# Kernel optimization log

Hardware: AMD Instinct MI355X
Metric: run time of the kernel (lower is better)

## Reference

```python
import jax, jax.numpy as jnp
import numpy as np
import math

HEADS = 32
GROUPS = 8
HEAD_DIM = 64
HIDDEN = 2048
B, S = 2, 2048


def _rope(x, freqs_cis):
    # x: (..., S, head_dim); freqs_cis: (S, head_dim) -> interleaved cos/sin pattern
    x_even = x[..., ::2]
    x_odd = x[..., 1::2]
    cos = freqs_cis[..., ::2]
    sin = freqs_cis[..., 1::2]
    r_even = x_even * cos - x_odd * sin
    r_odd = x_even * sin + x_odd * cos
    return jnp.stack([r_even, r_odd], axis=-1).reshape(x.shape)


def setup_inputs() -> dict:
    key = jax.random.key(0)
    ks = jax.random.split(key, 12)
    scale = 1.0 / math.sqrt(HIDDEN)
    x = jax.random.normal(ks[0], (B, S, HIDDEN), dtype=jnp.float32)
    freqs_cis = jax.random.uniform(ks[1], (S, HEAD_DIM), dtype=jnp.float32)
    causal = jnp.tril(jnp.ones((S, S), dtype=bool))
    mask = jnp.where(causal, 0.0, -1e9).astype(jnp.float32)
    kv_dims = HEAD_DIM * GROUPS
    wq = jax.random.normal(ks[2], (HIDDEN, HIDDEN), jnp.float32) * scale
    bq = jnp.zeros((HIDDEN,), jnp.float32)
    wk = jax.random.normal(ks[3], (kv_dims, HIDDEN), jnp.float32) * scale
    bk = jnp.zeros((kv_dims,), jnp.float32)
    wv = jax.random.normal(ks[4], (kv_dims, HIDDEN), jnp.float32) * scale
    bv = jnp.zeros((kv_dims,), jnp.float32)
    wo = jax.random.normal(ks[5], (HIDDEN, HIDDEN), jnp.float32) * scale
    bo = jnp.zeros((HIDDEN,), jnp.float32)
    return dict(x=x, freqs_cis=freqs_cis, mask=mask, wq=wq, bq=bq,
                wk=wk, bk=bk, wv=wv, bv=bv, wo=wo, bo=bo)


def reference(x, freqs_cis, mask, wq, bq, wk, bk, wv, bv, wo, bo):
    b, s, h = x.shape
    rep = HEADS // GROUPS
    q = x @ wq.T + bq                      # (B,S,H)
    k = x @ wk.T + bk                      # (B,S,G*hd)
    v = x @ wv.T + bv
    q = q.reshape(b, s, HEADS, HEAD_DIM).transpose(0, 2, 1, 3)   # (B,Hh,S,hd)
    k = k.reshape(b, s, GROUPS, HEAD_DIM).transpose(0, 2, 1, 3)  # (B,G,S,hd)
    v = v.reshape(b, s, GROUPS, HEAD_DIM).transpose(0, 2, 1, 3)
    q = _rope(q, freqs_cis)
    k = _rope(k, freqs_cis)
    # GQA: group q heads instead of materially repeating K/V
    qg = q.reshape(b, GROUPS, rep, s, HEAD_DIM)
    scores = jnp.einsum('bgrsd,bgtd->bgrst', qg, k) / math.sqrt(HEAD_DIM)
    scores = scores + mask                 # broadcast (S,S)
    attn = jax.nn.softmax(scores, axis=-1)
    out = jnp.einsum('bgrst,bgtd->bgrsd', attn, v)
    out = out.reshape(b, HEADS, s, HEAD_DIM).transpose(0, 2, 1, 3).reshape(b, s, h)
    return out @ wo.T + bo
```

## Files before the change

### kernel.cpp

```cpp
#include <hip/hip_runtime.h>

#define S_LEN 2048
#define HID   2048
#define NQH   32
#define NKV   8
#define HD    64

typedef __bf16 bf16x8 __attribute__((ext_vector_type(8)));
typedef __bf16 bf16x4 __attribute__((ext_vector_type(4)));
typedef float  f32x4  __attribute__((ext_vector_type(4)));

#define MFMA16(a, b, c) __builtin_amdgcn_mfma_f32_16x16x32_bf16(a, b, c, 0, 0, 0)

__device__ __forceinline__ void async_copy16(const void* g, void* l) {
  __builtin_amdgcn_global_load_lds(
      (const __attribute__((address_space(1))) unsigned int*)g,
      (__attribute__((address_space(3))) unsigned int*)l, 16, 0, 0);
}

__global__ void cast_all_k(const float* __restrict__ x,  const float* __restrict__ wq,
                           const float* __restrict__ wk, const float* __restrict__ wv,
                           const float* __restrict__ wo,
                           __bf16* __restrict__ xb,  __bf16* __restrict__ wqb,
                           __bf16* __restrict__ wkb, __bf16* __restrict__ wvb,
                           __bf16* __restrict__ wob) {
  int bid = blockIdx.x;
  const float* in; __bf16* out; int base;
  if (bid < 8192)       { in = x;  out = xb;  base = bid; }
  else if (bid < 12288) { in = wq; out = wqb; base = bid - 8192; }
  else if (bid < 13312) { in = wk; out = wkb; base = bid - 12288; }
  else if (bid < 14336) { in = wv; out = wvb; base = bid - 13312; }
  else                  { in = wo; out = wob; base = bid - 14336; }
  int i = (base * 256 + threadIdx.x) * 4;
  float4 v = *(const float4*)(in + i);
  bf16x4 o;
  o[0] = (__bf16)v.x; o[1] = (__bf16)v.y; o[2] = (__bf16)v.z; o[3] = (__bf16)v.w;
  *(bf16x4*)(out + i) = o;
}

__device__ __forceinline__ void gemm_core(const __bf16* __restrict__ A, const __bf16* __restrict__ B,
                                          int m0, int n0, int K,
                                          __bf16 (&Asm)[128][32], __bf16 (&Bsm)[128][32],
                                          f32x4 (&acc)[4][4]) {
  const int tid = threadIdx.x, wave = tid >> 6, lane = tid & 63;
  const int l15 = lane & 15, quad = lane >> 4;
  const int wr = wave >> 1, wc = wave & 1;
  const int lrow = lane >> 2, lcol = (lane & 3) * 8;

  const __bf16* ag = A + (size_t)(m0 + wave * 32 + lrow) * K + lcol;
  const __bf16* bg = B + (size_t)(n0 + wave * 32 + lrow) * K + lcol;
  __bf16* al = &Asm[wave * 32][0];
  __bf16* bl = &Bsm[wave * 32][0];
  const size_t rowstep = (size_t)16 * K;

  for (int kt = 0; kt < K; kt += 32) {
    __syncthreads();
    async_copy16(ag + kt, al);
    async_copy16(ag + kt + rowstep, al + 16 * 32);
    async_copy16(bg + kt, bl);
    async_copy16(bg + kt + rowstep, bl + 16 * 32);
    __syncthreads();
    bf16x8 af[4], bfr[4];
#pragma unroll
    for (int mt = 0; mt < 4; mt++)
      af[mt] = *(const bf16x8*)&Asm[wr * 64 + mt * 16 + l15][quad * 8];
#pragma unroll
    for (int nt = 0; nt < 4; nt++)
      bfr[nt] = *(const bf16x8*)&Bsm[wc * 64 + nt * 16 + l15][quad * 8];
#pragma unroll
    for (int mt = 0; mt < 4; mt++)
#pragma unroll
      for (int nt = 0; nt < 4; nt++)
        acc[mt][nt] = MFMA16(af[mt], bfr[nt], acc[mt][nt]);
  }
}

__global__ __launch_bounds__(256) void gemm_qkv_k(const __bf16* __restrict__ xb,
    const __bf16* __restrict__ wqb, const __bf16* __restrict__ wkb, const __bf16* __restrict__ wvb,
    const float* __restrict__ bq, const float* __restrict__ bk, const float* __restrict__ bv,
    const float* __restrict__ fr,
    __bf16* __restrict__ Qb, __bf16* __restrict__ Kb, __bf16* __restrict__ Vt) {
  __shared__ __align__(16) __bf16 Asm[128][32];
  __shared__ __align__(16) __bf16 Bsm[128][32];
  const int by = blockIdx.y;
  const int m0 = blockIdx.x * 128;
  const __bf16* B; const float* bias; int n0;
  int mode;
  if (by < 16)      { B = wqb; bias = bq; n0 = by * 128;        mode = 0; }
  else if (by < 20) { B = wkb; bias = bk; n0 = (by - 16) * 128; mode = 1; }
  else              { B = wvb; bias = bv; n0 = (by - 20) * 128; mode = 2; }

  f32x4 acc[4][4] = {};
  gemm_core(xb, B, m0, n0, HID, Asm, Bsm, acc);

  const int tid = threadIdx.x, wave = tid >> 6, lane = tid & 63;
  const int l15 = lane & 15, quad = lane >> 4;
  const int wr = wave >> 1, wc = wave & 1;

  if (mode == 2) {
#pragma unroll
    for (int nt = 0; nt < 4; nt++) {
      int col = n0 + wc * 64 + nt * 16 + l15;
      int g = col >> 6, d = col & 63;
      float bv2 = bias[col];
#pragma unroll
      for (int mt = 0; mt < 4; mt++) {
        int row = m0 + wr * 64 + mt * 16 + quad * 4;
        int b = row >> 11, s = row & 2047;
        bf16x4 o;
#pragma unroll
        for (int r = 0; r < 4; r++) o[r] = (__bf16)(acc[mt][nt][r] + bv2);
        *(bf16x4*)(Vt + (((size_t)(b * NKV + g) * HD + d)) * S_LEN + s) = o;
      }
    }
  } else {
    const float scale = (mode == 0) ? 0.125f * 1.44269504f : 1.0f;
    const int ldc = (mode == 0) ? HID : 512;
    __bf16* C = (mode == 0) ? Qb : Kb;
    const int dpar = l15 & 1;
#pragma unroll
    for (int nt = 0; nt < 4; nt++) {
      int col = n0 + wc * 64 + nt * 16 + l15;
      int d = col & 63;
      float bv2 = bias[col];
#pragma unroll
      for (int mt = 0; mt < 4; mt++) {
        int row = m0 + wr * 64 + mt * 16 + quad * 4;
        int s = row & 2047;
#pragma unroll
        for (int r = 0; r < 4; r++) {
          float v = acc[mt][nt][r] + bv2;
          float p = __shfl_xor(v, 1, 64);
          float f = fr[(size_t)(s + r) * HD + d];
          float fp = __shfl_xor(f, 1, 64);
          float o = dpar ? (p * f + v * fp) : (v * f - p * fp);
          C[(size_t)(row + r) * ldc + col] = (__bf16)(o * scale);
        }
      }
    }
  }
}

__global__ __launch_bounds__(256) void gemm_out_k(const __bf16* __restrict__ A,
    const __bf16* __restrict__ Bw, const float* __restrict__ bias, float* __restrict__ C) {
  __shared__ __align__(16) __bf16 Asm[128][32];
  __shared__ __align__(16) __bf16 Bsm[128][32];
  const int m0 = blockIdx.x * 128, n0 = blockIdx.y * 128;
  f32x4 acc[4][4] = {};
  gemm_core(A, Bw, m0, n0, HID, Asm, Bsm, acc);
  const int tid = threadIdx.x, wave = tid >> 6, lane = tid & 63;
  const int l15 = lane & 15, quad = lane >> 4;
  const int wr = wave >> 1, wc = wave & 1;
#pragma unroll
  for (int nt = 0; nt < 4; nt++) {
    int col = n0 + wc * 64 + nt * 16 + l15;
    float bv = bias[col];
#pragma unroll
    for (int mt = 0; mt < 4; mt++) {
      int row = m0 + wr * 64 + mt * 16 + quad * 4;
#pragma unroll
      for (int r = 0; r < 4; r++)
        C[(size_t)(row + r) * HID + col] = acc[mt][nt][r] + bv;
    }
  }
}

__global__ __launch_bounds__(256, 4) void flash_k(const __bf16* __restrict__ Q,
                                                  const __bf16* __restrict__ K,
                                                  const __bf16* __restrict__ Vt,
                                                  __bf16* __restrict__ O) {
  __shared__ __align__(64) __bf16 Ksm[64][64];
  __shared__ __align__(64) __bf16 Vsm[64][64];
  __shared__ __align__(64) __bf16 Psm[4][16][64];
  const int tid = threadIdx.x;
  const int wave = tid >> 6, lane = tid & 63;
  const int l15 = lane & 15, quad = lane >> 4;
  const int x7 = l15 & 7, l15h = l15 >> 3;
  const int bh = blockIdx.x;
  const int b = bh >> 5, h = bh & 31, g = h >> 2;

  const int srow = tid >> 2, sc = (tid & 3) * 16;
  const int r7 = srow & 7;
  const int w0 = (((sc >> 3))     ^ r7) * 8;
  const int w1 = (((sc >> 3) + 1) ^ r7) * 8;

  char* kbp = (char*)&Ksm[0][0];
  char* vbp = (char*)&Vsm[0][0];
  char* pbp = (char*)&Psm[0][0][0];
  int kr[2], pr[2], pw[4];
#pragma unroll
  for (int ks = 0; ks < 2; ks++) {
    kr[ks] = l15 * 128 + (((ks * 4 + quad) ^ x7) * 16);
    pr[ks] = wave * 2048 + kr[ks];
  }
#pragma unroll
  for (int nt = 0; nt < 4; nt++)
    pw[nt] = wave * 2048 + quad * 512 + x7 * 2 + (((2 * nt + l15h) ^ ((quad & 1) * 4)) * 16);

  bf16x8 ones;
#pragma unroll
  for (int j = 0; j < 8; j++) ones[j] = (__bf16)1.0f;

  const __bf16* kbase = K + ((size_t)b * S_LEN + srow) * (NKV * HD) + g * HD + sc;
  const __bf16* vbase = Vt + (((size_t)b * NKV + g) * HD + srow) * S_LEN + sc;

#pragma unroll 1
  for (int half = 0; half < 2; half++) {
    const int qt = half ? (31 - (int)blockIdx.y) : (int)blockIdx.y;
    const int wq0 = qt * 64 + wave * 16;

    const __bf16* qp = Q + ((size_t)(b * S_LEN + wq0 + l15)) * HID + h * HD + quad * 8;
    bf16x8 qf0 = *(const bf16x8*)qp;
    bf16x8 qf1 = *(const bf16x8*)(qp + 32);

    f32x4 acc[4] = {};
    f32x4 accs = {};

    const __bf16* kp = kbase;
    const __bf16* vp = vbase;
    uint4 k0 = *(const uint4*)kp, k1 = *(const uint4*)(kp + 8);
    uint4 v0 = *(const uint4*)vp, v1 = *(const uint4*)(vp + 8);

    for (int t = 0; t <= qt; t++) {
      const int kv0 = t * 64;
      __syncthreads();
      *(uint4*)&Ksm[srow][w0] = k0;
      *(uint4*)&Ksm[srow][w1] = k1;
      *(uint4*)&Vsm[srow][w0] = v0;
      *(uint4*)&Vsm[srow][w1] = v1;
      if (t < qt) {
        kp += 64 * NKV * HD;  vp += 64;
        k0 = *(const uint4*)kp; k1 = *(const uint4*)(kp + 8);
        v0 = *(const uint4*)vp; v1 = *(const uint4*)(vp + 8);
      }
      __syncthreads();

      if (kv0 > wq0 + 15) continue;

      bf16x8 kf[2][4];
#pragma unroll
      for (int ks = 0; ks < 2; ks++)
#pragma unroll
        for (int nt = 0; nt < 4; nt++)
          kf[ks][nt] = *(const bf16x8*)(kbp + (kr[ks] + nt * 2048));

      f32x4 sacc[4] = {};
#pragma unroll
      for (int nt = 0; nt < 4; nt++) {
        sacc[nt] = MFMA16(qf0, kf[0][nt], sacc[nt]);
        sacc[nt] = MFMA16(qf1, kf[1][nt], sacc[nt]);
      }
      const bool domask = (kv0 + 63 > wq0);
#pragma unroll
      for (int nt = 0; nt < 4; nt++) {
        int kv = kv0 + nt * 16 + l15;
        int qr = wq0 + quad * 4;
#pragma unroll
        for (int r = 0; r < 4; r++) {
          float p = __builtin_exp2f(sacc[nt][r]);
          if (domask && kv > qr + r) p = 0.f;
          *(__bf16*)(pbp + ((pw[nt] ^ (r << 4)) + r * 128)) = (__bf16)p;
        }
      }

#pragma unroll
      for (int ks = 0; ks < 2; ks++) {
        bf16x8 vf[4];
#pragma unroll
        for (int nt = 0; nt < 4; nt++)
          vf[nt] = *(const bf16x8*)(vbp + (kr[ks] + nt * 2048));
        bf16x8 pf = *(const bf16x8*)(pbp + pr[ks]);
        accs = MFMA16(pf, ones, accs);
#pragma unroll
        for (int nt = 0; nt < 4; nt++)
          acc[nt] = MFMA16(pf, vf[nt], acc[nt]);
      }
    }

    __bf16* op = O + ((size_t)(b * S_LEN + wq0 + quad * 4)) * HID + h * HD;
    float inv[4];
#pragma unroll
    for (int r = 0; r < 4; r++) inv[r] = 1.f / accs[r];
#pragma unroll
    for (int nt = 0; nt < 4; nt++)
#pragma unroll
      for (int r = 0; r < 4; r++)
        op[(size_t)r * HID + nt * 16 + l15] = (__bf16)(acc[nt][r] * inv[r]);
  }
}

extern "C" void kernel_launch(void* const* d_in, const int* in_sizes, int n_in,
                              void* d_out, int out_size, void* d_ws, size_t ws_size,
                              hipStream_t stream) {
  (void)in_sizes; (void)n_in; (void)out_size; (void)ws_size;
  const float* x  = (const float*)d_in[0];
  const float* fr = (const float*)d_in[1];
  const float* wq = (const float*)d_in[3];
  const float* bq = (const float*)d_in[4];
  const float* wk = (const float*)d_in[5];
  const float* bk = (const float*)d_in[6];
  const float* wv = (const float*)d_in[7];
  const float* bv = (const float*)d_in[8];
  const float* wo = (const float*)d_in[9];
  const float* bo = (const float*)d_in[10];
  float* out = (float*)d_out;
  char* ws = (char*)d_ws;

  __bf16* xb  = (__bf16*)(ws);
  __bf16* wqb = (__bf16*)(ws + ((size_t)16 << 20));
  __bf16* wkb = (__bf16*)(ws + ((size_t)24 << 20));
  __bf16* wvb = (__bf16*)(ws + ((size_t)26 << 20));
  __bf16* wob = (__bf16*)(ws + ((size_t)28 << 20));
  __bf16* Qb  = (__bf16*)(ws + ((size_t)36 << 20));
  __bf16* Kb  = (__bf16*)(ws + ((size_t)52 << 20));
  __bf16* Vtb = (__bf16*)(ws + ((size_t)60 << 20));
  __bf16* Ab  = (__bf16*)(ws + ((size_t)64 << 20));

  cast_all_k<<<18432, 256, 0, stream>>>(x, wq, wk, wv, wo, xb, wqb, wkb, wvb, wob);

  gemm_qkv_k<<<dim3(32, 24), 256, 0, stream>>>(xb, wqb, wkb, wvb, bq, bk, bv, fr, Qb, Kb, Vtb);

  flash_k<<<dim3(64, 16), 256, 0, stream>>>(Qb, Kb, Vtb, Ab);

  gemm_out_k<<<dim3(32, 16), 256, 0, stream>>>(Ab, wob, bo, out);
}
```

Before: 341.9 us.

## Triple-buffer GEMM loads with swizzled LDS and larger 256x128 tiles

Replaces the single-buffered 128x128x32 GEMM core with a three-stage async global-to-LDS pipeline using 256x128x64 tiles, 512-thread blocks, XOR-swizzled LDS columns to avoid bank conflicts, and s_setprio around the MFMA block. Both the QKV projection and output projection kernels use the new core, with halved grid in M. The aim is to hide global load latency behind MFMA work and reduce barrier overhead per K step. The risk is higher LDS use (about 144KB per block) limiting occupancy, and fewer blocks (384 and 256) against the CU count.

```diff
diff --git a/kernel.cpp b/kernel.cpp
--- a/kernel.cpp
+++ b/kernel.cpp
@@ -5,6 +5,10 @@
 #define NQH   32
 #define NKV   8
 #define HD    64
+
+#define BM 256
+#define BN 128
+#define BK 64
 
 typedef __bf16 bf16x8 __attribute__((ext_vector_type(8)));
 typedef __bf16 bf16x4 __attribute__((ext_vector_type(4)));
@@ -38,52 +42,88 @@
   *(bf16x4*)(out + i) = o;
 }
 
-__device__ __forceinline__ void gemm_core(const __bf16* __restrict__ A, const __bf16* __restrict__ B,
+__device__ __forceinline__ void gemm_pipe(const __bf16* __restrict__ A,
+                                          const __bf16* __restrict__ B,
                                           int m0, int n0, int K,
-                                          __bf16 (&Asm)[128][32], __bf16 (&Bsm)[128][32],
+                                          __bf16 (&As)[3][BM][BK],
+                                          __bf16 (&Bs)[3][BN][BK],
                                           f32x4 (&acc)[4][4]) {
   const int tid = threadIdx.x, wave = tid >> 6, lane = tid & 63;
   const int l15 = lane & 15, quad = lane >> 4;
   const int wr = wave >> 1, wc = wave & 1;
-  const int lrow = lane >> 2, lcol = (lane & 3) * 8;
-
-  const __bf16* ag = A + (size_t)(m0 + wave * 32 + lrow) * K + lcol;
-  const __bf16* bg = B + (size_t)(n0 + wave * 32 + lrow) * K + lcol;
-  __bf16* al = &Asm[wave * 32][0];
-  __bf16* bl = &Bsm[wave * 32][0];
-  const size_t rowstep = (size_t)16 * K;
-
-  for (int kt = 0; kt < K; kt += 32) {
-    __syncthreads();
-    async_copy16(ag + kt, al);
-    async_copy16(ag + kt + rowstep, al + 16 * 32);
-    async_copy16(bg + kt, bl);
-    async_copy16(bg + kt + rowstep, bl + 16 * 32);
-    __syncthreads();
-    bf16x8 af[4], bfr[4];
-#pragma unroll
-    for (int mt = 0; mt < 4; mt++)
-      af[mt] = *(const bf16x8*)&Asm[wr * 64 + mt * 16 + l15][quad * 8];
-#pragma unroll
-    for (int nt = 0; nt < 4; nt++)
-      bfr[nt] = *(const bf16x8*)&Bsm[wc * 64 + nt * 16 + l15][quad * 8];
-#pragma unroll
-    for (int mt = 0; mt < 4; mt++)
-#pragma unroll
-      for (int nt = 0; nt < 4; nt++)
-        acc[mt][nt] = MFMA16(af[mt], bfr[nt], acc[mt][nt]);
-  }
-}
-
-__global__ __launch_bounds__(256) void gemm_qkv_k(const __bf16* __restrict__ xb,
+
+  const int srow = lane >> 3;
+  const int scol = ((lane & 7) ^ srow) * 8;
+  const __bf16* ga = A + (size_t)(m0 + wave * 32 + srow) * K + scol;
+  const __bf16* gb = B + (size_t)(n0 + wave * 16 + srow) * K + scol;
+
+  const int c0 = ((quad)     ^ (l15 & 7)) * 8;
+  const int c1 = ((4 + quad) ^ (l15 & 7)) * 8;
+
+  const int NT = K / BK;
+
+#define STAGE(st, kt) do {                                                        \
+    _Pragma("unroll")                                                             \
+    for (int i = 0; i < 4; i++)                                                   \
+      async_copy16(ga + (kt) + (size_t)(i * 8) * K, &As[st][wave * 32 + i * 8][0]); \
+    _Pragma("unroll")                                                             \
+    for (int i = 0; i < 2; i++)                                                   \
+      async_copy16(gb + (kt) + (size_t)(i * 8) * K, &Bs[st][wave * 16 + i * 8][0]); \
+  } while (0)
+
+  STAGE(0, 0);
+  STAGE(1, BK);
+
+  int s = 0;
+  for (int t = 0; t < NT; t++) {
+    if (t + 1 < NT) asm volatile("s_waitcnt vmcnt(6) lgkmcnt(0)" ::: "memory");
+    else            asm volatile("s_waitcnt vmcnt(0) lgkmcnt(0)" ::: "memory");
+    __builtin_amdgcn_s_barrier();
+    asm volatile("" ::: "memory");
+
+    if (t + 2 < NT) {
+      int s2 = s + 2; if (s2 >= 3) s2 -= 3;
+      STAGE(s2, (t + 2) * BK);
+    }
+
+    const __bf16* a0 = &As[s][wr * 64][0];
+    const __bf16* b0 = &Bs[s][wc * 64][0];
+    bf16x8 af[2][4], bfr[2][4];
+#pragma unroll
+    for (int mt = 0; mt < 4; mt++) {
+      af[0][mt] = *(const bf16x8*)(a0 + (mt * 16 + l15) * BK + c0);
+      af[1][mt] = *(const bf16x8*)(a0 + (mt * 16 + l15) * BK + c1);
+    }
+#pragma unroll
+    for (int nt = 0; nt < 4; nt++) {
+      bfr[0][nt] = *(const bf16x8*)(b0 + (nt * 16 + l15) * BK + c0);
+      bfr[1][nt] = *(const bf16x8*)(b0 + (nt * 16 + l15) * BK + c1);
+    }
+
+    __builtin_amdgcn_s_setprio(1);
+#pragma unroll
+    for (int kk = 0; kk < 2; kk++)
+#pragma unroll
+      for (int mt = 0; mt < 4; mt++)
+#pragma unroll
+        for (int nt = 0; nt < 4; nt++)
+          acc[mt][nt] = MFMA16(af[kk][mt], bfr[kk][nt], acc[mt][nt]);
+    __builtin_amdgcn_s_setprio(0);
+
+    s = s + 1; if (s >= 3) s -= 3;
+  }
+#undef STAGE
+}
+
+__global__ __launch_bounds__(512, 2) void gemm_qkv_k(const __bf16* __restrict__ xb,
     const __bf16* __restrict__ wqb, const __bf16* __restrict__ wkb, const __bf16* __restrict__ wvb,
     const float* __restrict__ bq, const float* __restrict__ bk, const float* __restrict__ bv,
     const float* __restrict__ fr,
     __bf16* __restrict__ Qb, __bf16* __restrict__ Kb, __bf16* __restrict__ Vt) {
-  __shared__ __align__(16) __bf16 Asm[128][32];
-  __shared__ __align__(16) __bf16 Bsm[128][32];
+  __shared__ __align__(16) __bf16 As[3][BM][BK];
+  __shared__ __align__(16) __bf16 Bs[3][BN][BK];
   const int by = blockIdx.y;
-  const int m0 = blockIdx.x * 128;
+  const int m0 = blockIdx.x * BM;
   const __bf16* B; const float* bias; int n0;
   int mode;
   if (by < 16)      { B = wqb; bias = bq; n0 = by * 128;        mode = 0; }
@@ -91,7 +131,7 @@
   else              { B = wvb; bias = bv; n0 = (by - 20) * 128; mode = 2; }
 
   f32x4 acc[4][4] = {};
-  gemm_core(xb, B, m0, n0, HID, Asm, Bsm, acc);
+  gemm_pipe(xb, B, m0, n0, HID, As, Bs, acc);
 
   const int tid = threadIdx.x, wave = tid >> 6, lane = tid & 63;
   const int l15 = lane & 15, quad = lane >> 4;
@@ -106,11 +146,11 @@
 #pragma unroll
       for (int mt = 0; mt < 4; mt++) {
         int row = m0 + wr * 64 + mt * 16 + quad * 4;
-        int b = row >> 11, s = row & 2047;
+        int b = row >> 11, sI = row & 2047;
         bf16x4 o;
 #pragma unroll
         for (int r = 0; r < 4; r++) o[r] = (__bf16)(acc[mt][nt][r] + bv2);
-        *(bf16x4*)(Vt + (((size_t)(b * NKV + g) * HD + d)) * S_LEN + s) = o;
+        *(bf16x4*)(Vt + (((size_t)(b * NKV + g) * HD + d)) * S_LEN + sI) = o;
       }
     }
   } else {
@@ -126,12 +166,12 @@
 #pragma unroll
       for (int mt = 0; mt < 4; mt++) {
         int row = m0 + wr * 64 + mt * 16 + quad * 4;
-        int s = row & 2047;
+        int sI = row & 2047;
 #pragma unroll
         for (int r = 0; r < 4; r++) {
           float v = acc[mt][nt][r] + bv2;
           float p = __shfl_xor(v, 1, 64);
-          float f = fr[(size_t)(s + r) * HD + d];
+          float f = fr[(size_t)(sI + r) * HD + d];
           float fp = __shfl_xor(f, 1, 64);
           float o = dpar ? (p * f + v * fp) : (v * f - p * fp);
           C[(size_t)(row + r) * ldc + col] = (__bf16)(o * scale);
@@ -141,13 +181,13 @@
   }
 }
 
-__global__ __launch_bounds__(256) void gemm_out_k(const __bf16* __restrict__ A,
+__global__ __launch_bounds__(512, 2) void gemm_out_k(const __bf16* __restrict__ A,
     const __bf16* __restrict__ Bw, const float* __restrict__ bias, float* __restrict__ C) {
-  __shared__ __align__(16) __bf16 Asm[128][32];
-  __shared__ __align__(16) __bf16 Bsm[128][32];
-  const int m0 = blockIdx.x * 128, n0 = blockIdx.y * 128;
+  __shared__ __align__(16) __bf16 As[3][BM][BK];
+  __shared__ __align__(16) __bf16 Bs[3][BN][BK];
+  const int m0 = blockIdx.x * BM, n0 = blockIdx.y * BN;
   f32x4 acc[4][4] = {};
-  gemm_core(A, Bw, m0, n0, HID, Asm, Bsm, acc);
+  gemm_pipe(A, Bw, m0, n0, HID, As, Bs, acc);
   const int tid = threadIdx.x, wave = tid >> 6, lane = tid & 63;
   const int l15 = lane & 15, quad = lane >> 4;
   const int wr = wave >> 1, wc = wave & 1;
@@ -318,9 +358,9 @@
 
   cast_all_k<<<18432, 256, 0, stream>>>(x, wq, wk, wv, wo, xb, wqb, wkb, wvb, wob);
 
-  gemm_qkv_k<<<dim3(32, 24), 256, 0, stream>>>(xb, wqb, wkb, wvb, bq, bk, bv, fr, Qb, Kb, Vtb);
+  gemm_qkv_k<<<dim3(16, 24), 512, 0, stream>>>(xb, wqb, wkb, wvb, bq, bk, bv, fr, Qb, Kb, Vtb);
 
   flash_k<<<dim3(64, 16), 256, 0, stream>>>(Qb, Kb, Vtb, Ab);
 
-  gemm_out_k<<<dim3(32, 16), 256, 0, stream>>>(Ab, wob, bo, out);
-}
+  gemm_out_k<<<dim3(16, 16), 512, 0, stream>>>(Ab, wob, bo, out);
+}
```

Result: no change. 339.8 us (-0.6%).
